# Optimization experiments

Hardware: AMD Instinct MI355X
Metric: run time of the kernel (lower is better)

The kernel has to match this reference:

```python
import jax, jax.numpy as jnp
import numpy as np

B = 4096        # number of sets
MAX_N = 64      # max set size (matches max(n) in data)
DIM = 256       # per-element feature dim
W = 32          # weight_dim = sqrt(hidden_dim=1024)


def sinusoid_pe(length, dim):
    # standard transformer sinusoid PE: pe[p,2i]=sin(p/10000^(2i/dim)), pe[p,2i+1]=cos(...)
    pos = jnp.arange(length, dtype=jnp.float32)[:, None]
    i = jnp.arange(dim)[None, :]
    angle = pos / jnp.power(10000.0, (2.0 * (i // 2)).astype(jnp.float32) / dim)
    return jnp.where(i % 2 == 0, jnp.sin(angle), jnp.cos(angle))


def setup_inputs() -> dict:
    key = jax.random.key(0)
    ks = jax.random.split(key, 6)
    # ragged batch: alternating set sizes 32 and 64, 2048 each -> 196608 rows
    counts = np.tile(np.array([32, 64], dtype=np.int64), B // 2)
    batch = jnp.asarray(np.repeat(np.arange(B, dtype=np.int64), counts))
    N = int(counts.sum())
    x = jax.random.normal(ks[0], (N, DIM), dtype=jnp.float32)
    s = 1.0 / np.sqrt(DIM)
    Wk = jax.random.normal(ks[1], (W, DIM), dtype=jnp.float32) * s
    Wv = jax.random.normal(ks[2], (W, DIM), dtype=jnp.float32) * s
    Wq = jax.random.normal(ks[3], (W, DIM), dtype=jnp.float32) * s
    Wmap = jax.random.normal(ks[4], (DIM, W), dtype=jnp.float32) / np.sqrt(W)
    bmap = jax.random.normal(ks[5], (DIM,), dtype=jnp.float32) * 0.01
    return {"x": x, "batch": batch, "Wk": Wk, "Wv": Wv, "Wq": Wq, "Wmap": Wmap, "bmap": bmap}


def reference(x, batch, Wk, Wv, Wq, Wmap, bmap):
    N = x.shape[0]
    # set sizes and within-set positions (vectorized replacement of torch python loops)
    n = jax.ops.segment_sum(jnp.ones((N,), jnp.int32), batch, num_segments=B)
    ptr = jnp.concatenate([jnp.zeros((1,), jnp.int32), jnp.cumsum(n)])[:-1]
    pos_in_set = jnp.arange(N, dtype=jnp.int32) - ptr[batch]

    # --- Encoder ---
    xmat = jnp.zeros((B, MAX_N, DIM), x.dtype).at[batch, pos_in_set].set(x)
    mask = jnp.zeros((B, MAX_N), bool).at[batch, pos_in_set].set(True)
    pe = sinusoid_pe(MAX_N, DIM)                       # [MAX_N, DIM]
    xpos = xmat + pe[None]                             # [B, MAX_N, DIM]
    m = mask[..., None].astype(x.dtype)
    yk = jnp.einsum('bnd,wd->bnw', xpos, Wk) * m       # [B, MAX_N, W]
    yv = jnp.einsum('bnd,wd->bnw', xpos, Wv) * m
    # z_mat[b,i,j] = sum_n yv[b,n,i] * yk[b,n,j]
    z_mat = jnp.einsum('bnj,bni->bij', yk, yv)         # [B, W, W]

    # --- Decoder ---
    query = sinusoid_pe(MAX_N, DIM) @ Wq.T             # [MAX_N, W]
    decoded = jnp.einsum('mk,bkv->bmv', query, z_mat)  # [B, MAX_N, W]
    x_padded = decoded @ Wmap.T + bmap                 # [B, MAX_N, DIM]
    # unpad: gather valid rows back to flat ragged layout
    x_out = x_padded[batch, pos_in_set]                # [N, DIM]
    return (x_out, batch)
```

## Files before the change

kernel.cpp:

```cpp
#include <hip/hip_runtime.h>
#include <math.h>

#define N_SETS 4096

typedef _Float16 f16;
typedef __attribute__((ext_vector_type(8))) _Float16 f16x8;
typedef __attribute__((ext_vector_type(4))) _Float16 f16x4;
typedef __attribute__((ext_vector_type(4))) float     f32x4;

#define WS_PE    0
#define WS_QH    65536
#define WS_WKV   69632
#define WS_WMAPH 102400
#define WS_PEKV  118784
#define WS_PTR   135168

__global__ void k_aux1(const int* __restrict__ batch, float* __restrict__ out2,
                       int* __restrict__ ptr, int N, float* __restrict__ pe) {
    int blk = blockIdx.x;
    if (blk < 768) {
        int i = blk * 256 + threadIdx.x;
        if (i >= N) return;
        int b = batch[i];
        out2[i] = (float)b;
        if (i == 0 || batch[i - 1] != b) ptr[b] = i;
        if (i == N - 1) ptr[N_SETS] = N;
    } else {
        int idx = (blk - 768) * 256 + threadIdx.x;
        int p = idx >> 8, i = idx & 255;
        float e   = (float)(2 * (i / 2)) / 256.0f;
        float inv = powf(10000.0f, -e);
        float ang = (float)p * inv;
        pe[idx] = (i & 1) ? cosf(ang) : sinf(ang);
    }
}

__global__ void k_aux2(const float* __restrict__ Wk, const float* __restrict__ Wv,
                       const float* __restrict__ Wq, const float* __restrict__ Wmap,
                       const float* __restrict__ pe, f16* __restrict__ wkv,
                       f16* __restrict__ wmaph, float* __restrict__ pekv,
                       f16* __restrict__ qh) {
    int blk = blockIdx.x;
    if (blk < 96) {
        int idx = blk * 256 + threadIdx.x;
        if (idx < 16384) {
            int j = idx >> 8, d = idx & 255;
            float v = (j < 32) ? Wk[j * 256 + d] : Wv[(j - 32) * 256 + d];
            wkv[idx] = (f16)v;
        } else {
            int i2 = idx - 16384;
            wmaph[i2] = (f16)Wmap[i2];
        }
    } else {
        int idx = (blk - 96) * 256 + threadIdx.x;
        if (idx < 4096) {
            int pos = idx >> 6, j = idx & 63;
            const float* w  = (j < 32) ? (Wk + j * 256) : (Wv + (j - 32) * 256);
            const float* pr = pe + pos * 256;
            float s = 0.f;
            for (int d = 0; d < 256; d += 4) {
                float4 a = *(const float4*)(pr + d);
                float4 b = *(const float4*)(w + d);
                s += a.x * b.x + a.y * b.y + a.z * b.z + a.w * b.w;
            }
            pekv[idx] = s;
        } else if (idx < 6144) {
            int i2 = idx - 4096;
            int pos = i2 >> 5, k = i2 & 31;
            const float* pr = pe + pos * 256;
            const float* wr = Wq + k * 256;
            float s = 0.f;
            for (int d = 0; d < 256; d += 4) {
                float4 a = *(const float4*)(pr + d);
                float4 b = *(const float4*)(wr + d);
                s += a.x * b.x + a.y * b.y + a.z * b.z + a.w * b.w;
            }
            qh[i2] = (f16)s;
        }
    }
}

__global__ __launch_bounds__(256, 4) void k_main(
        const float* __restrict__ x,     const f16* __restrict__ wkv,
        const f16* __restrict__ wmaph,   const f16* __restrict__ qh,
        const float* __restrict__ pekv,  const float* __restrict__ bmap,
        const int* __restrict__ ptr,     float* __restrict__ out) {
    __shared__ char lds[31744];
    float* bsh = (float*)(lds + 30720);

    const int b    = blockIdx.x;
    const int t    = threadIdx.x;
    const int wv   = t >> 6;
    const int l15  = t & 15;
    const int lhi  = (t & 63) >> 4;
    const int s = ptr[b];
    const int n = ptr[b + 1] - s;

    {
        int m = t >> 2, v0 = (t & 3) * 8;
        f16x8 q8 = *(const f16x8*)(qh + m * 32 + v0);
        *(f16x8*)(lds + 24576 + ((m * 64 + v0 * 2) ^ ((m & 7) << 4))) = q8;
    }
    bsh[t] = bmap[t];
    #pragma unroll
    for (int i2 = 0; i2 < 4; ++i2) {
        int c = t + 256 * i2;
        int j = c >> 5, d0 = (c & 31) * 8;
        f16x8 w8 = *(const f16x8*)(wkv + j * 256 + d0);
        *(f16x8*)(lds + ((j * 512 + d0 * 2) ^ ((j & 7) << 4))) = w8;
    }
    f16x8 areg[8];
    {
        const int arow = 16 * wv + l15;
        if (arow < n) {
            const float* xr = x + (size_t)(s + arow) * 256 + lhi * 8;
            #pragma unroll
            for (int ks = 0; ks < 8; ++ks) {
                float4 a  = *(const float4*)(xr + ks * 32);
                float4 a2 = *(const float4*)(xr + ks * 32 + 4);
                f16x8 h;
                h[0]=(f16)a.x;  h[1]=(f16)a.y;  h[2]=(f16)a.z;  h[3]=(f16)a.w;
                h[4]=(f16)a2.x; h[5]=(f16)a2.y; h[6]=(f16)a2.z; h[7]=(f16)a2.w;
                areg[ks] = h;
            }
        } else {
            #pragma unroll
            for (int ks = 0; ks < 8; ++ks) {
                f16x8 h;
                #pragma unroll
                for (int ii = 0; ii < 8; ++ii) h[ii] = (f16)0.f;
                areg[ks] = h;
            }
        }
    }
    __syncthreads();

    #pragma unroll
    for (int pass = 0; pass < 2; ++pass) {
        f32x4 acc0 = {0.f,0.f,0.f,0.f}, acc1 = {0.f,0.f,0.f,0.f};
        if (16 * wv < n) {
            #pragma unroll
            for (int ks = 0; ks < 8; ++ks) {
                const int off = ks * 64 + lhi * 16;
                f16x8 b0 = *(const f16x8*)(lds + ((l15 * 512 + off) ^ ((l15 & 7) << 4)));
                f16x8 b1 = *(const f16x8*)(lds + (((16 + l15) * 512 + off) ^ ((l15 & 7) << 4)));
                acc0 = __builtin_amdgcn_mfma_f32_16x16x32_f16(areg[ks], b0, acc0, 0, 0, 0);
                acc1 = __builtin_amdgcn_mfma_f32_16x16x32_f16(areg[ks], b1, acc1, 0, 0, 0);
            }
        }
        const int row0 = 16 * wv + lhi * 4;
        #pragma unroll
        for (int nt = 0; nt < 2; ++nt) {
            const f32x4 A = nt ? acc1 : acc0;
            const int col = pass * 32 + 16 * nt + l15;
            f16x4 h4;
            #pragma unroll
            for (int q = 0; q < 4; ++q) {
                const int row = row0 + q;
                const float v = (row < n) ? (A[q] + pekv[row * 64 + col]) : 0.f;
                h4[q] = (f16)v;
            }
            *(f16x4*)(lds + 16384 + ((col * 128 + row0 * 2) ^ ((col & 7) << 4))) = h4;
        }
        __syncthreads();
        if (pass == 0) {
            #pragma unroll
            for (int i2 = 0; i2 < 4; ++i2) {
                int c = t + 256 * i2;
                int j = c >> 5, d0 = (c & 31) * 8;
                f16x8 w8 = *(const f16x8*)(wkv + (32 + j) * 256 + d0);
                *(f16x8*)(lds + ((j * 512 + d0 * 2) ^ ((j & 7) << 4))) = w8;
            }
            __syncthreads();
        }
    }

    {
        const int it = wv >> 1, jt = wv & 1;
        f32x4 zacc = {0.f,0.f,0.f,0.f};
        const int nks = (n + 31) >> 5;
        for (int ks = 0; ks < nks; ++ks) {
            const int r2 = ks * 64 + lhi * 16;
            f16x8 av = *(const f16x8*)(lds + 16384 + (((32 + 16 * it + l15) * 128 + r2) ^ ((l15 & 7) << 4)));
            f16x8 bk = *(const f16x8*)(lds + 16384 + (((16 * jt + l15) * 128 + r2) ^ ((l15 & 7) << 4)));
            zacc = __builtin_amdgcn_mfma_f32_16x16x32_f16(av, bk, zacc, 0, 0, 0);
        }
        #pragma unroll
        for (int i2 = 0; i2 < 4; ++i2) {
            int c = t + 256 * i2;
            int d = c >> 2, v0 = (c & 3) * 8;
            f16x8 w8 = *(const f16x8*)(wmaph + d * 32 + v0);
            *(f16x8*)(lds + ((d * 64 + v0 * 2) ^ ((d & 7) << 4))) = w8;
        }
        const int zc = 16 * jt + l15, zr0 = 16 * it + lhi * 4;
        f16x4 h4;
        #pragma unroll
        for (int q = 0; q < 4; ++q) h4[q] = (f16)zacc[q];
        *(f16x4*)(lds + 28672 + ((zc * 64 + zr0 * 2) ^ ((zc & 3) << 4))) = h4;
    }
    __syncthreads();

    if (16 * wv < n) {
        const int k2 = lhi * 16;
        f16x8 aq  = *(const f16x8*)(lds + 24576 + (((16 * wv + l15) * 64 + k2) ^ ((l15 & 7) << 4)));
        f16x8 bz0 = *(const f16x8*)(lds + 28672 + ((l15 * 64 + k2) ^ ((l15 & 3) << 4)));
        f16x8 bz1 = *(const f16x8*)(lds + 28672 + (((16 + l15) * 64 + k2) ^ ((l15 & 3) << 4)));
        f32x4 dd0 = {0.f,0.f,0.f,0.f}, dd1 = {0.f,0.f,0.f,0.f};
        dd0 = __builtin_amdgcn_mfma_f32_16x16x32_f16(aq, bz0, dd0, 0, 0, 0);
        dd1 = __builtin_amdgcn_mfma_f32_16x16x32_f16(aq, bz1, dd1, 0, 0, 0);
        #pragma unroll
        for (int q = 0; q < 4; ++q) {
            const int m = 16 * wv + lhi * 4 + q;
            *(f16*)(lds + 16384 + ((m * 64 + l15 * 2) ^ ((m & 7) << 4)))      = (f16)dd0[q];
            *(f16*)(lds + 16384 + ((m * 64 + 32 + l15 * 2) ^ ((m & 7) << 4))) = (f16)dd1[q];
        }
    }
    __syncthreads();

    if (16 * wv < n) {
        const int k2 = lhi * 16;
        f16x8 ad = *(const f16x8*)(lds + 16384 + (((16 * wv + l15) * 64 + k2) ^ ((l15 & 7) << 4)));
        const int row0 = 16 * wv + lhi * 4;
        float* orow = out + (size_t)s * 256;
        #pragma unroll
        for (int nt = 0; nt < 16; ++nt) {
            const int dcol = 16 * nt + l15;
            f16x8 bw = *(const f16x8*)(lds + ((dcol * 64 + k2) ^ ((l15 & 7) << 4)));
            f32x4 o = {0.f,0.f,0.f,0.f};
            o = __builtin_amdgcn_mfma_f32_16x16x32_f16(ad, bw, o, 0, 0, 0);
            const float bb = bsh[dcol];
            #pragma unroll
            for (int q = 0; q < 4; ++q) {
                const int row = row0 + q;
                if (row < n) orow[(size_t)row * 256 + dcol] = o[q] + bb;
            }
        }
    }
}

extern "C" void kernel_launch(void* const* d_in, const int* in_sizes, int n_in,
                              void* d_out, int out_size, void* d_ws, size_t ws_size,
                              hipStream_t stream) {
    const float* x    = (const float*)d_in[0];
    const int*   batch= (const int*)  d_in[1];
    const float* Wk   = (const float*)d_in[2];
    const float* Wv   = (const float*)d_in[3];
    const float* Wq   = (const float*)d_in[4];
    const float* Wmap = (const float*)d_in[5];
    const float* bmap = (const float*)d_in[6];
    float* out = (float*)d_out;

    const int N = in_sizes[1];
    float* pe    = (float*)((char*)d_ws + WS_PE);
    f16*   qh    = (f16*)  ((char*)d_ws + WS_QH);
    f16*   wkv   = (f16*)  ((char*)d_ws + WS_WKV);
    f16*   wmaph = (f16*)  ((char*)d_ws + WS_WMAPH);
    float* pekv  = (float*)((char*)d_ws + WS_PEKV);
    int*   ptr   = (int*)  ((char*)d_ws + WS_PTR);
    float* out2  = out + (size_t)N * 256;

    k_aux1<<<832, 256, 0, stream>>>(batch, out2, ptr, N, pe);
    k_aux2<<<120, 256, 0, stream>>>(Wk, Wv, Wq, Wmap, pe, wkv, wmaph, pekv, qh);
    k_main<<<N_SETS, 256, 0, stream>>>(x, wkv, wmaph, qh, pekv, bmap, ptr, out);
}
```

Baseline: 125.4 us.

## Process eight sets per block with resident weights and prefetched x rows

The main kernel now loops over eight sets per block. All of Wk/Wv and Wmap are loaded into LDS once per block, and the query and PE fragments are kept in registers. The next set's x rows are prefetched into registers while the current set is computed. The positional encoding is added to x in fp16 before the projection, replacing the precomputed fp32 PE·W correction, and all 64 k/v columns are computed in one pass. This amortises weight staging and hides global load latency, at the cost of more LDS and registers (occupancy hint lowered to 2), only 512 blocks, and slightly different rounding.

```diff
diff --git a/kernel.cpp b/kernel.cpp
--- a/kernel.cpp
+++ b/kernel.cpp
@@ -2,6 +2,8 @@
 #include <math.h>
 
 #define N_SETS 4096
+#define SETS_PER_BLOCK 8
+#define GRID_MAIN (N_SETS / SETS_PER_BLOCK)
 
 typedef _Float16 f16;
 typedef __attribute__((ext_vector_type(8))) _Float16 f16x8;
@@ -12,8 +14,8 @@
 #define WS_QH    65536
 #define WS_WKV   69632
 #define WS_WMAPH 102400
-#define WS_PEKV  118784
-#define WS_PTR   135168
+#define WS_PEH   118784
+#define WS_PTR   151552
 
 __global__ void k_aux1(const int* __restrict__ batch, float* __restrict__ out2,
                        int* __restrict__ ptr, int N, float* __restrict__ pe) {
@@ -38,7 +40,7 @@
 __global__ void k_aux2(const float* __restrict__ Wk, const float* __restrict__ Wv,
                        const float* __restrict__ Wq, const float* __restrict__ Wmap,
                        const float* __restrict__ pe, f16* __restrict__ wkv,
-                       f16* __restrict__ wmaph, float* __restrict__ pekv,
+                       f16* __restrict__ wmaph, f16* __restrict__ peh,
                        f16* __restrict__ qh) {
     int blk = blockIdx.x;
     if (blk < 96) {
@@ -51,77 +53,92 @@
             int i2 = idx - 16384;
             wmaph[i2] = (f16)Wmap[i2];
         }
+    } else if (blk < 160) {
+        int idx = (blk - 96) * 256 + threadIdx.x;
+        peh[idx] = (f16)pe[idx];
     } else {
-        int idx = (blk - 96) * 256 + threadIdx.x;
-        if (idx < 4096) {
-            int pos = idx >> 6, j = idx & 63;
-            const float* w  = (j < 32) ? (Wk + j * 256) : (Wv + (j - 32) * 256);
-            const float* pr = pe + pos * 256;
-            float s = 0.f;
-            for (int d = 0; d < 256; d += 4) {
-                float4 a = *(const float4*)(pr + d);
-                float4 b = *(const float4*)(w + d);
-                s += a.x * b.x + a.y * b.y + a.z * b.z + a.w * b.w;
-            }
-            pekv[idx] = s;
-        } else if (idx < 6144) {
-            int i2 = idx - 4096;
-            int pos = i2 >> 5, k = i2 & 31;
-            const float* pr = pe + pos * 256;
-            const float* wr = Wq + k * 256;
-            float s = 0.f;
-            for (int d = 0; d < 256; d += 4) {
-                float4 a = *(const float4*)(pr + d);
-                float4 b = *(const float4*)(wr + d);
-                s += a.x * b.x + a.y * b.y + a.z * b.z + a.w * b.w;
-            }
-            qh[i2] = (f16)s;
-        }
-    }
-}
-
-__global__ __launch_bounds__(256, 4) void k_main(
+        int idx = (blk - 160) * 256 + threadIdx.x;
+        int pos = idx >> 5, k = idx & 31;
+        const float* pr = pe + pos * 256;
+        const float* wr = Wq + k * 256;
+        float s = 0.f;
+        for (int d = 0; d < 256; d += 4) {
+            float4 a = *(const float4*)(pr + d);
+            float4 b = *(const float4*)(wr + d);
+            s += a.x * b.x + a.y * b.y + a.z * b.z + a.w * b.w;
+        }
+        qh[idx] = (f16)s;
+    }
+}
+
+__global__ __launch_bounds__(256, 2) void k_main(
         const float* __restrict__ x,     const f16* __restrict__ wkv,
         const f16* __restrict__ wmaph,   const f16* __restrict__ qh,
-        const float* __restrict__ pekv,  const float* __restrict__ bmap,
+        const f16* __restrict__ peh,     const float* __restrict__ bmap,
         const int* __restrict__ ptr,     float* __restrict__ out) {
-    __shared__ char lds[31744];
-    float* bsh = (float*)(lds + 30720);
-
-    const int b    = blockIdx.x;
+    __shared__ char lds[59392];
+
     const int t    = threadIdx.x;
     const int wv   = t >> 6;
     const int l15  = t & 15;
     const int lhi  = (t & 63) >> 4;
-    const int s = ptr[b];
-    const int n = ptr[b + 1] - s;
-
-    {
-        int m = t >> 2, v0 = (t & 3) * 8;
-        f16x8 q8 = *(const f16x8*)(qh + m * 32 + v0);
-        *(f16x8*)(lds + 24576 + ((m * 64 + v0 * 2) ^ ((m & 7) << 4))) = q8;
-    }
-    bsh[t] = bmap[t];
-    #pragma unroll
-    for (int i2 = 0; i2 < 4; ++i2) {
+    const int arow = 16 * wv + l15;
+
+    int pv[SETS_PER_BLOCK + 1];
+    #pragma unroll
+    for (int i = 0; i <= SETS_PER_BLOCK; ++i)
+        pv[i] = ptr[blockIdx.x * SETS_PER_BLOCK + i];
+
+    #pragma unroll
+    for (int i2 = 0; i2 < 8; ++i2) {
         int c = t + 256 * i2;
         int j = c >> 5, d0 = (c & 31) * 8;
         f16x8 w8 = *(const f16x8*)(wkv + j * 256 + d0);
         *(f16x8*)(lds + ((j * 512 + d0 * 2) ^ ((j & 7) << 4))) = w8;
     }
-    f16x8 areg[8];
+    #pragma unroll
+    for (int i2 = 0; i2 < 4; ++i2) {
+        int c = t + 256 * i2;
+        int d = c >> 2, v0 = (c & 3) * 8;
+        f16x8 w8 = *(const f16x8*)(wmaph + d * 32 + v0);
+        *(f16x8*)(lds + 32768 + ((d * 64 + v0 * 2) ^ ((d & 7) << 4))) = w8;
+    }
+    f16x8 pef[8];
+    #pragma unroll
+    for (int ks = 0; ks < 8; ++ks)
+        pef[ks] = *(const f16x8*)(peh + arow * 256 + ks * 32 + lhi * 8);
+    const f16x8 qreg = *(const f16x8*)(qh + arow * 32 + lhi * 8);
+    float bm[16];
+    #pragma unroll
+    for (int nt = 0; nt < 16; ++nt) bm[nt] = bmap[16 * nt + l15];
+
+    float4 xf[16];
     {
-        const int arow = 16 * wv + l15;
+        const int s0 = pv[0], n0 = pv[1] - pv[0];
+        if (arow < n0) {
+            const float* xr = x + (size_t)(s0 + arow) * 256 + lhi * 8;
+            #pragma unroll
+            for (int ks = 0; ks < 8; ++ks) {
+                xf[2 * ks]     = *(const float4*)(xr + ks * 32);
+                xf[2 * ks + 1] = *(const float4*)(xr + ks * 32 + 4);
+            }
+        }
+    }
+    __syncthreads();
+
+    for (int si = 0; si < SETS_PER_BLOCK; ++si) {
+        const int s = pv[si], n = pv[si + 1] - s;
+        const int n32 = (n + 31) & ~31;
+
+        f16x8 areg[8];
         if (arow < n) {
-            const float* xr = x + (size_t)(s + arow) * 256 + lhi * 8;
-            #pragma unroll
-            for (int ks = 0; ks < 8; ++ks) {
-                float4 a  = *(const float4*)(xr + ks * 32);
-                float4 a2 = *(const float4*)(xr + ks * 32 + 4);
+            #pragma unroll
+            for (int ks = 0; ks < 8; ++ks) {
+                float4 a = xf[2 * ks], a2 = xf[2 * ks + 1];
                 f16x8 h;
                 h[0]=(f16)a.x;  h[1]=(f16)a.y;  h[2]=(f16)a.z;  h[3]=(f16)a.w;
                 h[4]=(f16)a2.x; h[5]=(f16)a2.y; h[6]=(f16)a2.z; h[7]=(f16)a2.w;
-                areg[ks] = h;
+                areg[ks] = h + pef[ks];
             }
         } else {
             #pragma unroll
@@ -132,109 +149,99 @@
                 areg[ks] = h;
             }
         }
-    }
-    __syncthreads();
-
-    #pragma unroll
-    for (int pass = 0; pass < 2; ++pass) {
-        f32x4 acc0 = {0.f,0.f,0.f,0.f}, acc1 = {0.f,0.f,0.f,0.f};
+        if (si + 1 < SETS_PER_BLOCK) {
+            const int s1 = pv[si + 1], n1 = pv[si + 2] - pv[si + 1];
+            if (arow < n1) {
+                const float* xr = x + (size_t)(s1 + arow) * 256 + lhi * 8;
+                #pragma unroll
+                for (int ks = 0; ks < 8; ++ks) {
+                    xf[2 * ks]     = *(const float4*)(xr + ks * 32);
+                    xf[2 * ks + 1] = *(const float4*)(xr + ks * 32 + 4);
+                }
+            }
+        }
+
+        if (16 * wv < n32) {
+            f32x4 acc[4];
+            #pragma unroll
+            for (int nt = 0; nt < 4; ++nt) acc[nt] = (f32x4){0.f, 0.f, 0.f, 0.f};
+            #pragma unroll
+            for (int ks = 0; ks < 8; ++ks) {
+                #pragma unroll
+                for (int nt = 0; nt < 4; ++nt) {
+                    f16x8 bf = *(const f16x8*)(lds +
+                        (((16 * nt + l15) * 512 + ks * 64 + lhi * 16) ^ ((l15 & 7) << 4)));
+                    acc[nt] = __builtin_amdgcn_mfma_f32_16x16x32_f16(areg[ks], bf, acc[nt], 0, 0, 0);
+                }
+            }
+            const int row0 = 16 * wv + lhi * 4;
+            #pragma unroll
+            for (int nt = 0; nt < 4; ++nt) {
+                const int col = 16 * nt + l15;
+                f16x4 h4;
+                #pragma unroll
+                for (int q = 0; q < 4; ++q) h4[q] = (f16)acc[nt][q];
+                *(f16x4*)(lds + 49152 + ((col * 128 + row0 * 2) ^ ((col & 7) << 4))) = h4;
+            }
+        }
+        __syncthreads();
+
+        {
+            const int it = wv >> 1, jt = wv & 1;
+            f32x4 zacc = {0.f, 0.f, 0.f, 0.f};
+            const int nks = n32 >> 5;
+            for (int ks = 0; ks < nks; ++ks) {
+                const int r2 = ks * 64 + lhi * 16;
+                f16x8 av = *(const f16x8*)(lds + 49152 +
+                    (((32 + 16 * it + l15) * 128 + r2) ^ ((l15 & 7) << 4)));
+                f16x8 bk = *(const f16x8*)(lds + 49152 +
+                    (((16 * jt + l15) * 128 + r2) ^ ((l15 & 7) << 4)));
+                zacc = __builtin_amdgcn_mfma_f32_16x16x32_f16(av, bk, zacc, 0, 0, 0);
+            }
+            const int zc = 16 * jt + l15, zr0 = 16 * it + lhi * 4;
+            f16x4 h4;
+            #pragma unroll
+            for (int q = 0; q < 4; ++q) h4[q] = (f16)zacc[q];
+            *(f16x4*)(lds + 57344 + ((zc * 64 + zr0 * 2) ^ ((zc & 3) << 4))) = h4;
+        }
+        __syncthreads();
+
         if (16 * wv < n) {
-            #pragma unroll
-            for (int ks = 0; ks < 8; ++ks) {
-                const int off = ks * 64 + lhi * 16;
-                f16x8 b0 = *(const f16x8*)(lds + ((l15 * 512 + off) ^ ((l15 & 7) << 4)));
-                f16x8 b1 = *(const f16x8*)(lds + (((16 + l15) * 512 + off) ^ ((l15 & 7) << 4)));
-                acc0 = __builtin_amdgcn_mfma_f32_16x16x32_f16(areg[ks], b0, acc0, 0, 0, 0);
-                acc1 = __builtin_amdgcn_mfma_f32_16x16x32_f16(areg[ks], b1, acc1, 0, 0, 0);
-            }
-        }
-        const int row0 = 16 * wv + lhi * 4;
-        #pragma unroll
-        for (int nt = 0; nt < 2; ++nt) {
-            const f32x4 A = nt ? acc1 : acc0;
-            const int col = pass * 32 + 16 * nt + l15;
-            f16x4 h4;
+            const int k2 = lhi * 16;
+            f16x8 bz0 = *(const f16x8*)(lds + 57344 + ((l15 * 64 + k2) ^ ((l15 & 3) << 4)));
+            f16x8 bz1 = *(const f16x8*)(lds + 57344 + (((16 + l15) * 64 + k2) ^ ((l15 & 3) << 4)));
+            f32x4 dd0 = {0.f, 0.f, 0.f, 0.f}, dd1 = {0.f, 0.f, 0.f, 0.f};
+            dd0 = __builtin_amdgcn_mfma_f32_16x16x32_f16(qreg, bz0, dd0, 0, 0, 0);
+            dd1 = __builtin_amdgcn_mfma_f32_16x16x32_f16(qreg, bz1, dd1, 0, 0, 0);
             #pragma unroll
             for (int q = 0; q < 4; ++q) {
-                const int row = row0 + q;
-                const float v = (row < n) ? (A[q] + pekv[row * 64 + col]) : 0.f;
-                h4[q] = (f16)v;
-            }
-            *(f16x4*)(lds + 16384 + ((col * 128 + row0 * 2) ^ ((col & 7) << 4))) = h4;
-        }
-        __syncthreads();
-        if (pass == 0) {
-            #pragma unroll
-            for (int i2 = 0; i2 < 4; ++i2) {
-                int c = t + 256 * i2;
-                int j = c >> 5, d0 = (c & 31) * 8;
-                f16x8 w8 = *(const f16x8*)(wkv + (32 + j) * 256 + d0);
-                *(f16x8*)(lds + ((j * 512 + d0 * 2) ^ ((j & 7) << 4))) = w8;
-            }
-            __syncthreads();
-        }
-    }
-
-    {
-        const int it = wv >> 1, jt = wv & 1;
-        f32x4 zacc = {0.f,0.f,0.f,0.f};
-        const int nks = (n + 31) >> 5;
-        for (int ks = 0; ks < nks; ++ks) {
-            const int r2 = ks * 64 + lhi * 16;
-            f16x8 av = *(const f16x8*)(lds + 16384 + (((32 + 16 * it + l15) * 128 + r2) ^ ((l15 & 7) << 4)));
-            f16x8 bk = *(const f16x8*)(lds + 16384 + (((16 * jt + l15) * 128 + r2) ^ ((l15 & 7) << 4)));
-            zacc = __builtin_amdgcn_mfma_f32_16x16x32_f16(av, bk, zacc, 0, 0, 0);
-        }
-        #pragma unroll
-        for (int i2 = 0; i2 < 4; ++i2) {
-            int c = t + 256 * i2;
-            int d = c >> 2, v0 = (c & 3) * 8;
-            f16x8 w8 = *(const f16x8*)(wmaph + d * 32 + v0);
-            *(f16x8*)(lds + ((d * 64 + v0 * 2) ^ ((d & 7) << 4))) = w8;
-        }
-        const int zc = 16 * jt + l15, zr0 = 16 * it + lhi * 4;
-        f16x4 h4;
-        #pragma unroll
-        for (int q = 0; q < 4; ++q) h4[q] = (f16)zacc[q];
-        *(f16x4*)(lds + 28672 + ((zc * 64 + zr0 * 2) ^ ((zc & 3) << 4))) = h4;
-    }
-    __syncthreads();
-
-    if (16 * wv < n) {
-        const int k2 = lhi * 16;
-        f16x8 aq  = *(const f16x8*)(lds + 24576 + (((16 * wv + l15) * 64 + k2) ^ ((l15 & 7) << 4)));
-        f16x8 bz0 = *(const f16x8*)(lds + 28672 + ((l15 * 64 + k2) ^ ((l15 & 3) << 4)));
-        f16x8 bz1 = *(const f16x8*)(lds + 28672 + (((16 + l15) * 64 + k2) ^ ((l15 & 3) << 4)));
-        f32x4 dd0 = {0.f,0.f,0.f,0.f}, dd1 = {0.f,0.f,0.f,0.f};
-        dd0 = __builtin_amdgcn_mfma_f32_16x16x32_f16(aq, bz0, dd0, 0, 0, 0);
-        dd1 = __builtin_amdgcn_mfma_f32_16x16x32_f16(aq, bz1, dd1, 0, 0, 0);
-        #pragma unroll
-        for (int q = 0; q < 4; ++q) {
-            const int m = 16 * wv + lhi * 4 + q;
-            *(f16*)(lds + 16384 + ((m * 64 + l15 * 2) ^ ((m & 7) << 4)))      = (f16)dd0[q];
-            *(f16*)(lds + 16384 + ((m * 64 + 32 + l15 * 2) ^ ((m & 7) << 4))) = (f16)dd1[q];
-        }
-    }
-    __syncthreads();
-
-    if (16 * wv < n) {
-        const int k2 = lhi * 16;
-        f16x8 ad = *(const f16x8*)(lds + 16384 + (((16 * wv + l15) * 64 + k2) ^ ((l15 & 7) << 4)));
-        const int row0 = 16 * wv + lhi * 4;
-        float* orow = out + (size_t)s * 256;
-        #pragma unroll
-        for (int nt = 0; nt < 16; ++nt) {
-            const int dcol = 16 * nt + l15;
-            f16x8 bw = *(const f16x8*)(lds + ((dcol * 64 + k2) ^ ((l15 & 7) << 4)));
-            f32x4 o = {0.f,0.f,0.f,0.f};
-            o = __builtin_amdgcn_mfma_f32_16x16x32_f16(ad, bw, o, 0, 0, 0);
-            const float bb = bsh[dcol];
-            #pragma unroll
-            for (int q = 0; q < 4; ++q) {
-                const int row = row0 + q;
-                if (row < n) orow[(size_t)row * 256 + dcol] = o[q] + bb;
-            }
-        }
+                const int m = 16 * wv + lhi * 4 + q;
+                *(f16*)(lds + 49152 + ((m * 64 + l15 * 2) ^ ((m & 7) << 4)))            = (f16)dd0[q];
+                *(f16*)(lds + 49152 + ((m * 64 + (16 + l15) * 2) ^ ((m & 7) << 4)))     = (f16)dd1[q];
+            }
+        }
+        __syncthreads();
+
+        if (16 * wv < n) {
+            const int k2 = lhi * 16;
+            f16x8 ad = *(const f16x8*)(lds + 49152 +
+                (((16 * wv + l15) * 64 + k2) ^ ((l15 & 7) << 4)));
+            const int row0 = 16 * wv + lhi * 4;
+            float* orow = out + (size_t)s * 256;
+            #pragma unroll
+            for (int nt = 0; nt < 16; ++nt) {
+                const int dcol = 16 * nt + l15;
+                f16x8 bw = *(const f16x8*)(lds + 32768 + ((dcol * 64 + k2) ^ ((l15 & 7) << 4)));
+                f32x4 o = {0.f, 0.f, 0.f, 0.f};
+                o = __builtin_amdgcn_mfma_f32_16x16x32_f16(ad, bw, o, 0, 0, 0);
+                #pragma unroll
+                for (int q = 0; q < 4; ++q) {
+                    const int row = row0 + q;
+                    if (row < n) orow[(size_t)row * 256 + dcol] = o[q] + bm[nt];
+                }
+            }
+        }
+        __syncthreads();
     }
 }
 
@@ -255,11 +262,11 @@
     f16*   qh    = (f16*)  ((char*)d_ws + WS_QH);
     f16*   wkv   = (f16*)  ((char*)d_ws + WS_WKV);
     f16*   wmaph = (f16*)  ((char*)d_ws + WS_WMAPH);
-    float* pekv  = (float*)((char*)d_ws + WS_PEKV);
+    f16*   peh   = (f16*)  ((char*)d_ws + WS_PEH);
     int*   ptr   = (int*)  ((char*)d_ws + WS_PTR);
     float* out2  = out + (size_t)N * 256;
 
     k_aux1<<<832, 256, 0, stream>>>(batch, out2, ptr, N, pe);
-    k_aux2<<<120, 256, 0, stream>>>(Wk, Wv, Wq, Wmap, pe, wkv, wmaph, pekv, qh);
-    k_main<<<N_SETS, 256, 0, stream>>>(x, wkv, wmaph, qh, pekv, bmap, ptr, out);
-}
+    k_aux2<<<168, 256, 0, stream>>>(Wk, Wv, Wq, Wmap, pe, wkv, wmaph, peh, qh);
+    k_main<<<GRID_MAIN, 256, 0, stream>>>(x, wkv, wmaph, qh, peh, bmap, ptr, out);
+}
```

Result: faster. 115.2 us (-8.2%).
